# Optimization experiments

Hardware: AMD Instinct MI355X
Metric: run time of the kernel (lower is better)

## Reference

```python
import jax, jax.numpy as jnp
import numpy as np

N = 50000      # num nodes
E = 800000     # num edges (before self loops)
F_IN = 128     # fea_size
D = 128        # g_dim_per_layer[i]
H = 4          # heads
C = D // H     # out_channels per head
NEG_SLOPE = 0.2  # PyG GATConv default leaky_relu slope


def setup_inputs() -> dict:
    key = jax.random.key(0)
    ks = jax.random.split(key, 20)
    inp = {
        "x": jax.random.normal(ks[0], (N, F_IN), dtype=jnp.float32),
        "edge_index": jax.random.randint(ks[1], (2, E), 0, N, dtype=jnp.int32),
        "w0": jax.random.normal(ks[2], (F_IN, D), dtype=jnp.float32) * 0.05,
        "b0": jnp.zeros((D,), dtype=jnp.float32),
    }
    for i in (1, 2, 3):
        k = 4 * i
        inp[f"w{i}"] = jax.random.normal(ks[k], (D, D), dtype=jnp.float32) * 0.05
        inp[f"a_src{i}"] = jax.random.normal(ks[k + 1], (H, C), dtype=jnp.float32) * 0.1
        inp[f"a_dst{i}"] = jax.random.normal(ks[k + 2], (H, C), dtype=jnp.float32) * 0.1
        inp[f"b{i}"] = jnp.zeros((D,), dtype=jnp.float32)
    return inp


def _gat_layer(x, src, dst, w, a_src, a_dst, b):
    # PyG GATConv (eval mode, dropout inactive, add_self_loops already applied)
    n = x.shape[0]
    xp = (x @ w).reshape(n, H, C)                       # [N,H,C]
    al_s = jnp.einsum("nhc,hc->nh", xp, a_src)          # [N,H]
    al_d = jnp.einsum("nhc,hc->nh", xp, a_dst)          # [N,H]
    e = jax.nn.leaky_relu(al_s[src] + al_d[dst], NEG_SLOPE)  # [E',H]
    # softmax over incoming edges of each destination node
    m = jax.ops.segment_max(e, dst, num_segments=n)
    e = jnp.exp(e - m[dst])
    s = jax.ops.segment_sum(e, dst, num_segments=n)
    alpha = e / s[dst]                                  # [E',H]
    msg = alpha[:, :, None] * xp[src]                   # [E',H,C]
    out = jax.ops.segment_sum(msg, dst, num_segments=n)  # [N,H,C]
    return out.reshape(n, H * C) + b


def reference(x, edge_index, w0, b0, w1, a_src1, a_dst1, b1,
              w2, a_src2, a_dst2, b2, w3, a_src3, a_dst3, b3):
    n = x.shape[0]
    loops = jnp.arange(n, dtype=edge_index.dtype)
    ei = jnp.concatenate([edge_index, jnp.stack([loops, loops])], axis=1)
    src, dst = ei[0], ei[1]  # messages flow src -> dst (PyG convention)

    h = x @ w0 + b0
    h = jax.nn.relu(h + _gat_layer(h, src, dst, w1, a_src1, a_dst1, b1))
    h = jax.nn.relu(h + _gat_layer(h, src, dst, w2, a_src2, a_dst2, b2))
    return _gat_layer(h, src, dst, w3, a_src3, a_dst3, b3)
```

## Files before the change

kernel.cpp:

```cpp
#include <hip/hip_runtime.h>

#define F 128
#define HEADS 4
#define NEG 0.2f
#define CAP 128
#define CAPP 136
#define CB 6144

typedef unsigned short u16;
typedef unsigned int u32;
typedef __attribute__((ext_vector_type(8))) unsigned short us8;
typedef __attribute__((ext_vector_type(8))) short short8;
typedef __attribute__((ext_vector_type(4))) float f32x4;

__device__ __forceinline__ float bf2f(u16 u) {
  union { u32 i; float f; } v; v.i = ((u32)u) << 16; return v.f;
}
__device__ __forceinline__ float bflo(u32 p) {
  union { u32 i; float f; } v; v.i = p << 16; return v.f;
}
__device__ __forceinline__ float bfhi(u32 p) {
  union { u32 i; float f; } v; v.i = p & 0xFFFF0000u; return v.f;
}
__device__ __forceinline__ u16 f2bf(float f) {
  union { u32 i; float f; } v; v.f = f;
  if (((v.i >> 23) & 0xFF) == 0xFF) return 0;
  u32 r = v.i + 0x7FFF + ((v.i >> 16) & 1);
  return (u16)(r >> 16);
}
__device__ __forceinline__ float sane(float f) {
  union { u32 i; float f; } v; v.f = f;
  return (((v.i >> 23) & 0xFF) == 0xFF) ? 0.f : f;
}
__device__ __forceinline__ u16 bfsane(u16 u) {
  return (((u >> 7) & 0xFF) == 0xFF) ? (u16)0 : u;
}

__device__ __forceinline__ bool detect_f32_wave(const u16* __restrict__ p) {
  int lane = threadIdx.x & 63;
  const us8* q = (const us8*)p + lane * 4;
  int c = 0;
  #pragma unroll
  for (int k = 0; k < 4; k++) {
    us8 v = q[k];
    #pragma unroll
    for (int j = 0; j < 8; j++) { unsigned e = (v[j] >> 7) & 0xFF; c += (e >= 0xF8); }
  }
  #pragma unroll
  for (int off = 32; off; off >>= 1) c += __shfl_xor(c, off);
  return c > 4;
}

__global__ __launch_bounds__(256) void fill_const_bf16(u16* __restrict__ p, u16 v, int n) {
  int i = blockIdx.x * blockDim.x + threadIdx.x;
  if (i < n) p[i] = v;
}

__global__ __launch_bounds__(256) void setup(
    const void* w0, const void* w1, const void* w2, const void* w3,
    const void* b0, const void* b1, const void* b2, const void* b3,
    const void* as1, const void* ad1, const void* as2, const void* ad2,
    const void* as3, const void* ad3,
    u16* __restrict__ wsz, float* __restrict__ par,
    int* __restrict__ flg, int* __restrict__ gcur) {
  bool f32 = detect_f32_wave((const u16*)w0);
  int blk = blockIdx.x, tid = threadIdx.x;
  if (blk < 32) {
    int idx = blk * 256 + tid;
    int layer = idx >> 11;
    int rest  = idx & 2047;
    int lane = rest & 63;
    int ts   = rest >> 6;
    int s = ts & 3, t = ts >> 2;
    int kbase = s * 32 + (lane >> 4) * 8;
    int nn    = t * 16 + (lane & 15);
    const void* W = (layer == 0) ? w0 : (layer == 1) ? w1 : (layer == 2) ? w2 : w3;
    us8 o;
    #pragma unroll
    for (int j = 0; j < 8; j++) {
      int off = (kbase + j) * F + nn;
      o[j] = f32 ? f2bf(sane(((const float*)W)[off])) : bfsane(((const u16*)W)[off]);
    }
    *(us8*)(wsz + (size_t)idx * 8) = o;
  } else if (blk < 37) {
    int t = (blk - 32) * 256 + tid;
    if (t < 1280) {
      const void* tab[10] = {b0, b1, b2, b3, as1, ad1, as2, ad2, as3, ad3};
      const void* src = tab[t >> 7];
      int idx = t & 127;
      float v = f32 ? ((const float*)src)[idx] : bf2f(((const u16*)src)[idx]);
      par[t] = sane(v);
    }
  } else {
    gcur[tid] = 0;
    if (tid == 0) flg[0] = f32 ? 1 : 0;
  }
}

__global__ __launch_bounds__(256) void bucket_scatter(const int* __restrict__ ei,
                                                      int* __restrict__ gcur,
                                                      int2* __restrict__ ebuf,
                                                      int E, int E2, int n) {
  __shared__ int lcnt[256];
  __shared__ int gbase[256];
  int tid = threadIdx.x;
  lcnt[tid] = 0;
  __syncthreads();
  int srcv[16], dstv[16], rnk[16];
  #pragma unroll
  for (int i = 0; i < 16; i++) {
    int e = blockIdx.x * 4096 + i * 256 + tid;
    rnk[i] = -1;
    if (e < E2) {
      int src, dst;
      if (e < E) { src = ei[e]; dst = ei[E + e]; }
      else       { src = dst = e - E; }
      if ((unsigned)dst < (unsigned)n) {
        srcv[i] = src; dstv[i] = dst;
        rnk[i] = atomicAdd(&lcnt[dst >> 8], 1);
      }
    }
  }
  __syncthreads();
  int c = lcnt[tid];
  gbase[tid] = c ? atomicAdd(&gcur[tid], c) : 0;
  __syncthreads();
  #pragma unroll
  for (int i = 0; i < 16; i++) {
    if (rnk[i] >= 0) {
      int b = dstv[i] >> 8;
      int slot = gbase[b] + rnk[i];
      if (slot < CB) ebuf[(size_t)b * CB + slot] = make_int2(srcv[i], dstv[i]);
    }
  }
}

__global__ __launch_bounds__(256) void bucket_fill(const int* __restrict__ gcur,
                                                   const int2* __restrict__ ebuf,
                                                   int* __restrict__ rp,
                                                   int* __restrict__ col, int n) {
  __shared__ int sc[256];
  __shared__ int ncnt[256];
  __shared__ int nofs[256];
  __shared__ int wsums[4];
  __shared__ int total_s;
  int b = blockIdx.x, tid = threadIdx.x, lane = tid & 63, wv = tid >> 6;

  int v = min(gcur[tid], CB);
  int x = v;
  #pragma unroll
  for (int off = 1; off < 64; off <<= 1) {
    int t = __shfl_up(x, off);
    if (lane >= off) x += t;
  }
  if (lane == 63) wsums[wv] = x;
  __syncthreads();
  int add = 0;
  for (int w = 0; w < wv; w++) add += wsums[w];
  sc[tid] = add + x - v;
  if (tid == 255) total_s = add + x;
  __syncthreads();

  int tot = min(gcur[b], CB);
  int colbase = sc[b];
  const int2* eb = ebuf + (size_t)b * CB;
  ncnt[tid] = 0;
  __syncthreads();
  for (int j = tid; j < tot; j += 256) atomicAdd(&ncnt[eb[j].y & 255], 1);
  __syncthreads();
  v = ncnt[tid];
  x = v;
  #pragma unroll
  for (int off = 1; off < 64; off <<= 1) {
    int t = __shfl_up(x, off);
    if (lane >= off) x += t;
  }
  if (lane == 63) wsums[wv] = x;
  __syncthreads();
  add = 0;
  for (int w = 0; w < wv; w++) add += wsums[w];
  nofs[tid] = add + x - v;
  int node = (b << 8) + tid;
  if (node < n) rp[node] = colbase + nofs[tid];
  if (b == 0 && tid == 0) rp[n] = total_s;
  __syncthreads();
  ncnt[tid] = 0;
  __syncthreads();
  for (int j = tid; j < tot; j += 256) {
    int2 e = eb[j];
    int ln = e.y & 255;
    int r = atomicAdd(&ncnt[ln], 1);
    col[colbase + nofs[ln] + r] = e.x;
  }
}

__global__ __launch_bounds__(128) void gemm_mfma(
    const void* __restrict__ A, const u16* __restrict__ wszL,
    const float* __restrict__ biasc, const float* __restrict__ avec,
    u16* __restrict__ Cm, float* __restrict__ al_s, float* __restrict__ al_d,
    const int* __restrict__ flgp, int nrows, int a_src) {
  int tid = threadIdx.x, wv = tid >> 6, lane = tid & 63;
  int quad = lane >> 4, l15 = lane & 15;
  int m0 = blockIdx.x * 32 + wv * 16;
  int mrow = m0 + l15;
  int ml = mrow < nrows ? mrow : (nrows - 1);

  float asv[8], adv[8];
  if (avec) {
    #pragma unroll
    for (int t = 0; t < 8; t++) {
      asv[t] = avec[t * 16 + l15];
      adv[t] = avec[128 + t * 16 + l15];
    }
  }

  short8 af[4];
  if (a_src && flgp[0]) {
    const float* ar = (const float*)A + (size_t)ml * F;
    #pragma unroll
    for (int s = 0; s < 4; s++) {
      float4 u = *(const float4*)(ar + s * 32 + quad * 8);
      float4 v = *(const float4*)(ar + s * 32 + quad * 8 + 4);
      short8 p;
      p[0] = (short)f2bf(sane(u.x)); p[1] = (short)f2bf(sane(u.y));
      p[2] = (short)f2bf(sane(u.z)); p[3] = (short)f2bf(sane(u.w));
      p[4] = (short)f2bf(sane(v.x)); p[5] = (short)f2bf(sane(v.y));
      p[6] = (short)f2bf(sane(v.z)); p[7] = (short)f2bf(sane(v.w));
      af[s] = p;
    }
  } else {
    const u16* ar = (const u16*)A + (size_t)ml * F;
    #pragma unroll
    for (int s = 0; s < 4; s++) af[s] = *(const short8*)(ar + s * 32 + quad * 8);
  }

  f32x4 acc[8];
  #pragma unroll
  for (int t = 0; t < 8; t++) acc[t] = (f32x4){0.f, 0.f, 0.f, 0.f};
  #pragma unroll
  for (int s = 0; s < 4; s++) {
    #pragma unroll
    for (int t = 0; t < 8; t++) {
      short8 bf = *(const short8*)(wszL + (size_t)(((t << 2) | s) * 64 + lane) * 8);
      acc[t] = __builtin_amdgcn_mfma_f32_16x16x32_bf16(af[s], bf, acc[t], 0, 0, 0);
    }
  }

  float ps[4][4], pd[4][4];
  if (avec) {
    #pragma unroll
    for (int r = 0; r < 4; r++)
      #pragma unroll
      for (int h = 0; h < 4; h++) { ps[r][h] = 0.f; pd[r][h] = 0.f; }
  }

  #pragma unroll
  for (int t = 0; t < 8; t++) {
    int cc = t * 16 + l15;
    float b = biasc ? biasc[cc] : 0.f;
    int h = t >> 1;
    #pragma unroll
    for (int r = 0; r < 4; r++) {
      float v = sane(acc[t][r] + b);
      int row = m0 + quad * 4 + r;
      if (row < nrows) Cm[(size_t)row * F + cc] = f2bf(v);
      if (avec) { ps[r][h] += v * asv[t]; pd[r][h] += v * adv[t]; }
    }
  }

  if (avec) {
    #pragma unroll
    for (int r = 0; r < 4; r++)
      #pragma unroll
      for (int h = 0; h < 4; h++) {
        float a = ps[r][h], d = pd[r][h];
        #pragma unroll
        for (int off = 1; off < 16; off <<= 1) {
          a += __shfl_xor(a, off);
          d += __shfl_xor(d, off);
        }
        ps[r][h] = a; pd[r][h] = d;
      }
    if (l15 == 0) {
      #pragma unroll
      for (int r = 0; r < 4; r++) {
        int row = m0 + quad * 4 + r;
        if (row < nrows) {
          float4 vs = {sane(ps[r][0]), sane(ps[r][1]), sane(ps[r][2]), sane(ps[r][3])};
          float4 vd = {sane(pd[r][0]), sane(pd[r][1]), sane(pd[r][2]), sane(pd[r][3])};
          ((float4*)al_s)[row] = vs;
          ((float4*)al_d)[row] = vd;
        }
      }
    }
  }
}

__global__ __launch_bounds__(256) void gat_aggregate(
    const u16* __restrict__ xp, const float* __restrict__ al_s,
    const float* __restrict__ al_d, const int* __restrict__ row_ptr,
    const int* __restrict__ col, const float* __restrict__ biasc,
    u16* __restrict__ hio, const int* __restrict__ flgp,
    int n, int E2, int mode) {
  __shared__ int   sb[4][2][CAP];
  __shared__ float wb[4][2][4][CAPP];
  int tid = threadIdx.x;
  int wv = tid >> 6, lane = tid & 63;
  int half = lane >> 5, hl = lane & 31;
  int node = blockIdx.x * 8 + wv * 2 + half;
  bool active = node < n;
  int beg = 0, end = 0;
  float ald_[4] = {0.f, 0.f, 0.f, 0.f};
  if (active) {
    beg = row_ptr[node]; end = row_ptr[node + 1];
    if (beg < 0) beg = 0; if (beg > E2) beg = E2;
    if (end < beg) end = beg; if (end > E2) end = E2;
    float4 qd = ((const float4*)al_d)[node];
    ald_[0] = qd.x; ald_[1] = qd.y; ald_[2] = qd.z; ald_[3] = qd.w;
  }
  int deg = end - beg;
  int ch = hl * 4, head = hl >> 3;
  u32 cb = (u32)hl * 8;
  const char* xpb = (const char*)xp;
  float a0 = 0.f, a1 = 0.f, a2 = 0.f, a3 = 0.f;

  if (deg <= CAP) {
    float er[4][4];
    float m4[4] = {-1e30f, -1e30f, -1e30f, -1e30f};
    #pragma unroll
    for (int it = 0; it < 4; it++) {
      int jj = hl + it * 32;
      if (jj < deg) {
        int src = col[beg + jj];
        if ((unsigned)src >= (unsigned)n) src = node;
        sb[wv][half][jj] = src;
        float4 q = ((const float4*)al_s)[src];
        float as_[4] = {q.x, q.y, q.z, q.w};
        #pragma unroll
        for (int h = 0; h < 4; h++) {
          float e = as_[h] + ald_[h];
          e = (e > 0.f) ? e : NEG * e;
          er[it][h] = e;
          m4[h] = fmaxf(m4[h], e);
        }
      }
    }
    #pragma unroll
    for (int off = 16; off; off >>= 1)
      #pragma unroll
      for (int h = 0; h < 4; h++) m4[h] = fmaxf(m4[h], __shfl_xor(m4[h], off));
    float s4[4] = {0.f, 0.f, 0.f, 0.f};
    #pragma unroll
    for (int it = 0; it < 4; it++) {
      int jj = hl + it * 32;
      if (jj < deg) {
        #pragma unroll
        for (int h = 0; h < 4; h++) {
          float w = __expf(er[it][h] - m4[h]);
          s4[h] += w;
          wb[wv][half][h][jj] = w;
        }
      }
    }
    #pragma unroll
    for (int off = 16; off; off >>= 1)
      #pragma unroll
      for (int h = 0; h < 4; h++) s4[h] += __shfl_xor(s4[h], off);
    float inv = (s4[head] > 0.f) ? 1.f / s4[head] : 0.f;
    __asm__ volatile("s_waitcnt lgkmcnt(0)" ::: "memory");
    const int* srow = sb[wv][half];
    const float* wrow = wb[wv][half][head];
    int j = 0;
    for (; j + 4 <= deg; j += 4) {
      int4 sa = *(const int4*)(srow + j);
      float4 wa = *(const float4*)(wrow + j);
      uint2 p0 = *(const uint2*)(xpb + (((u32)sa.x << 8) + cb));
      uint2 p1 = *(const uint2*)(xpb + (((u32)sa.y << 8) + cb));
      uint2 p2 = *(const uint2*)(xpb + (((u32)sa.z << 8) + cb));
      uint2 p3 = *(const uint2*)(xpb + (((u32)sa.w << 8) + cb));
      a0 += wa.x * bflo(p0.x) + wa.y * bflo(p1.x) + wa.z * bflo(p2.x) + wa.w * bflo(p3.x);
      a1 += wa.x * bfhi(p0.x) + wa.y * bfhi(p1.x) + wa.z * bfhi(p2.x) + wa.w * bfhi(p3.x);
      a2 += wa.x * bflo(p0.y) + wa.y * bflo(p1.y) + wa.z * bflo(p2.y) + wa.w * bflo(p3.y);
      a3 += wa.x * bfhi(p0.y) + wa.y * bfhi(p1.y) + wa.z * bfhi(p2.y) + wa.w * bfhi(p3.y);
    }
    for (; j < deg; j++) {
      int s0 = srow[j];
      float w0 = wrow[j];
      uint2 p0 = *(const uint2*)(xpb + (((u32)s0 << 8) + cb));
      a0 += w0 * bflo(p0.x); a1 += w0 * bfhi(p0.x);
      a2 += w0 * bflo(p0.y); a3 += w0 * bfhi(p0.y);
    }
    a0 *= inv; a1 *= inv; a2 *= inv; a3 *= inv;
  } else {
    float m = -1.0e30f, s = 0.f;
    for (int j = beg; j < end; ++j) {
      int src = col[j];
      if ((unsigned)src >= (unsigned)n) continue;
      float e = al_s[src * 4 + head] + ald_[head];
      e = (e > 0.f) ? e : NEG * e;
      float mn = fmaxf(m, e);
      float scale = __expf(m - mn);
      float w = __expf(e - mn);
      uint2 pv = *(const uint2*)(xpb + (((u32)src << 8) + cb));
      s = s * scale + w;
      a0 = a0 * scale + w * bflo(pv.x);
      a1 = a1 * scale + w * bfhi(pv.x);
      a2 = a2 * scale + w * bflo(pv.y);
      a3 = a3 * scale + w * bfhi(pv.y);
      m = mn;
    }
    float inv = (s > 0.f) ? 1.f / s : 0.f;
    a0 *= inv; a1 *= inv; a2 *= inv; a3 *= inv;
  }

  if (!active) return;
  float4 b4 = *(const float4*)(biasc + ch);
  float o0 = sane(a0) + b4.x, o1 = sane(a1) + b4.y;
  float o2 = sane(a2) + b4.z, o3 = sane(a3) + b4.w;
  size_t o = (size_t)node * F + ch;
  if (mode == 0) {
    uint2 hv = *(const uint2*)(hio + o);
    o0 = fmaxf(bflo(hv.x) + o0, 0.f);
    o1 = fmaxf(bfhi(hv.x) + o1, 0.f);
    o2 = fmaxf(bflo(hv.y) + o2, 0.f);
    o3 = fmaxf(bfhi(hv.y) + o3, 0.f);
    uint2 st;
    st.x = ((u32)f2bf(sane(o1)) << 16) | (u32)f2bf(sane(o0));
    st.y = ((u32)f2bf(sane(o3)) << 16) | (u32)f2bf(sane(o2));
    *(uint2*)(hio + o) = st;
  } else {
    if (flgp[0]) {
      float4 st = {sane(o0), sane(o1), sane(o2), sane(o3)};
      *(float4*)((float*)hio + o) = st;
    } else {
      uint2 st;
      st.x = ((u32)f2bf(sane(o1)) << 16) | (u32)f2bf(sane(o0));
      st.y = ((u32)f2bf(sane(o3)) << 16) | (u32)f2bf(sane(o2));
      *(uint2*)(hio + o) = st;
    }
  }
}

extern "C" void kernel_launch(void* const* d_in, const int* in_sizes, int n_in,
                              void* d_out, int out_size, void* d_ws, size_t ws_size,
                              hipStream_t stream) {
  const int* ei = (const int*)d_in[1];

  const int N  = in_sizes[0] / F;
  const int E  = in_sizes[1] / 2;
  const int E2 = E + N;
  const int NB = (N + 255) >> 8;

  uintptr_t base = ((uintptr_t)d_ws + 255) & ~(uintptr_t)255;
  size_t off_par = 0;
  size_t off_flg = off_par + (size_t)1536 * 4;
  size_t off_wsz = off_flg + 256;
  size_t off_xp  = off_wsz + (size_t)65536 * 2;
  size_t off_als = off_xp  + (size_t)N * F * 2;
  size_t off_ald = off_als + (size_t)N * HEADS * 4;
  size_t off_gc  = off_ald + (size_t)N * HEADS * 4;
  size_t off_rp  = off_gc  + 1024;
  size_t off_col = off_rp  + (size_t)(N + 1) * 4;
  size_t off_eb  = (off_col + (size_t)E2 * 4 + 255) & ~(size_t)255;
  size_t need    = off_eb + (size_t)NB * CB * 8 + 512 + ((uintptr_t)d_ws & 255);

  if (ws_size < need) {
    fill_const_bf16<<<(out_size + 255) / 256, 256, 0, stream>>>(
        (u16*)d_out, (u16)0x4316, out_size);
    return;
  }

  float* par   = (float*)(base + off_par);
  int* flg     = (int*)(base + off_flg);
  u16* wsz     = (u16*)(base + off_wsz);
  u16* xp      = (u16*)(base + off_xp);
  float* al_s  = (float*)(base + off_als);
  float* al_d  = (float*)(base + off_ald);
  int* gcur    = (int*)(base + off_gc);
  int* row_ptr = (int*)(base + off_rp);
  int* col     = (int*)(base + off_col);
  int2* ebuf   = (int2*)(base + off_eb);

  float* bc[4];
  for (int l = 0; l < 4; ++l) bc[l] = par + (size_t)l * 128;
  float* avec[3];
  for (int l = 0; l < 3; ++l) avec[l] = par + 512 + (size_t)l * 256;

  u16* hio = (u16*)d_out;

  setup<<<38, 256, 0, stream>>>(
      d_in[2], d_in[4], d_in[8], d_in[12],
      d_in[3], d_in[7], d_in[11], d_in[15],
      d_in[5], d_in[6], d_in[9], d_in[10], d_in[13], d_in[14],
      wsz, par, flg, gcur);

  bucket_scatter<<<(E2 + 4095) / 4096, 256, 0, stream>>>(ei, gcur, ebuf, E, E2, N);
  bucket_fill<<<NB, 256, 0, stream>>>(gcur, ebuf, row_ptr, col, N);

  const int GB = (N + 31) / 32;
  gemm_mfma<<<GB, 128, 0, stream>>>(d_in[0], wsz, bc[0], nullptr, hio,
                                    al_s, al_d, flg, N, 1);

  for (int l = 0; l < 3; ++l) {
    gemm_mfma<<<GB, 128, 0, stream>>>(hio, wsz + (size_t)(l + 1) * 16384, nullptr,
                                      avec[l], xp, al_s, al_d, flg, N, 0);
    gat_aggregate<<<(N + 7) / 8, 256, 0, stream>>>(
        xp, al_s, al_d, row_ptr, col, bc[l + 1], hio, flg, N, E2, (l < 2) ? 0 : 1);
  }
}
```

Before: 324.9 us.

## Fuse graph build with GEMMs, fold attention vectors into MFMA, prefetch gather

Precomputes W·a_src and W·a_dst per layer in setup so the attention logits come from an extra MFMA column tile instead of a shuffle reduction in the GEMM epilogue. Runs the edge bucket scatter and the first projection GEMM in one launch, and the CSR fill and the layer-1 GEMM in another, so independent work overlaps and fewer kernels are launched. The aggregation inner loop also software-prefetches the next four neighbor rows. The cost is heavier setup work, plus logits rounded through bf16 weight vectors and possible load imbalance inside the merged grids.

```diff
diff --git a/kernel.cpp b/kernel.cpp
--- a/kernel.cpp
+++ b/kernel.cpp
@@ -61,8 +61,9 @@
     const void* b0, const void* b1, const void* b2, const void* b3,
     const void* as1, const void* ad1, const void* as2, const void* ad2,
     const void* as3, const void* ad3,
-    u16* __restrict__ wsz, float* __restrict__ par,
+    u16* __restrict__ wsz, u16* __restrict__ avf, float* __restrict__ par,
     int* __restrict__ flg, int* __restrict__ gcur) {
+  __shared__ float vv[8][128];
   bool f32 = detect_f32_wave((const u16*)w0);
   int blk = blockIdx.x, tid = threadIdx.x;
   if (blk < 32) {
@@ -91,16 +92,112 @@
       float v = f32 ? ((const float*)src)[idx] : bf2f(((const u16*)src)[idx]);
       par[t] = sane(v);
     }
-  } else {
+  } else if (blk == 37) {
     gcur[tid] = 0;
     if (tid == 0) flg[0] = f32 ? 1 : 0;
-  }
-}
-
-__global__ __launch_bounds__(256) void bucket_scatter(const int* __restrict__ ei,
-                                                      int* __restrict__ gcur,
-                                                      int2* __restrict__ ebuf,
-                                                      int E, int E2, int n) {
+  } else {
+    int l = blk - 38;
+    const void* W   = (l == 0) ? w1 : (l == 1) ? w2 : w3;
+    const void* asp = (l == 0) ? as1 : (l == 1) ? as2 : as3;
+    const void* adp = (l == 0) ? ad1 : (l == 1) ? ad2 : ad3;
+    for (int e = tid; e < 1024; e += 256) {
+      int vec = e >> 7, k = e & 127;
+      int h = vec & 3;
+      const void* av = (vec < 4) ? asp : adp;
+      float sum = 0.f;
+      for (int c = 0; c < 32; c++) {
+        int col = h * 32 + c;
+        float wv_ = f32 ? ((const float*)W)[k * F + col] : bf2f(((const u16*)W)[k * F + col]);
+        float aa  = f32 ? ((const float*)av)[col]        : bf2f(((const u16*)av)[col]);
+        sum += sane(wv_) * sane(aa);
+      }
+      vv[vec][k] = sane(sum);
+    }
+    __syncthreads();
+    int s = tid >> 6, lane = tid & 63;
+    int quad = lane >> 4, l15 = lane & 15;
+    int kbase = s * 32 + quad * 8;
+    us8 o;
+    #pragma unroll
+    for (int j = 0; j < 8; j++)
+      o[j] = (l15 < 8) ? f2bf(vv[l15][kbase + j]) : (u16)0;
+    *(us8*)(avf + (((size_t)l * 4 + s) * 64 + lane) * 8) = o;
+  }
+}
+
+__device__ __forceinline__ void gemm_tile(
+    int m0, int lane, const void* __restrict__ A, int f32in,
+    const u16* __restrict__ wszL, const float* __restrict__ biasc,
+    const u16* __restrict__ avfL, u16* __restrict__ Cm,
+    float* __restrict__ al_s, float* __restrict__ al_d, int nrows) {
+  int quad = lane >> 4, l15 = lane & 15;
+  int mrow = m0 + l15;
+  int ml = mrow < nrows ? mrow : (nrows - 1);
+  short8 af[4];
+  if (f32in) {
+    const float* ar = (const float*)A + (size_t)ml * F;
+    #pragma unroll
+    for (int s = 0; s < 4; s++) {
+      float4 u = *(const float4*)(ar + s * 32 + quad * 8);
+      float4 v = *(const float4*)(ar + s * 32 + quad * 8 + 4);
+      short8 p;
+      p[0] = (short)f2bf(sane(u.x)); p[1] = (short)f2bf(sane(u.y));
+      p[2] = (short)f2bf(sane(u.z)); p[3] = (short)f2bf(sane(u.w));
+      p[4] = (short)f2bf(sane(v.x)); p[5] = (short)f2bf(sane(v.y));
+      p[6] = (short)f2bf(sane(v.z)); p[7] = (short)f2bf(sane(v.w));
+      af[s] = p;
+    }
+  } else {
+    const u16* ar = (const u16*)A + (size_t)ml * F;
+    #pragma unroll
+    for (int s = 0; s < 4; s++) af[s] = *(const short8*)(ar + s * 32 + quad * 8);
+  }
+
+  f32x4 acc[8];
+  #pragma unroll
+  for (int t = 0; t < 8; t++) acc[t] = (f32x4){0.f, 0.f, 0.f, 0.f};
+  f32x4 accL = (f32x4){0.f, 0.f, 0.f, 0.f};
+
+  #pragma unroll
+  for (int s = 0; s < 4; s++) {
+    short8 bfr[8];
+    #pragma unroll
+    for (int t = 0; t < 8; t++)
+      bfr[t] = *(const short8*)(wszL + (size_t)(((t << 2) | s) * 64 + lane) * 8);
+    if (avfL) {
+      short8 av = *(const short8*)(avfL + (size_t)(s * 64 + lane) * 8);
+      accL = __builtin_amdgcn_mfma_f32_16x16x32_bf16(af[s], av, accL, 0, 0, 0);
+    }
+    #pragma unroll
+    for (int t = 0; t < 8; t++)
+      acc[t] = __builtin_amdgcn_mfma_f32_16x16x32_bf16(af[s], bfr[t], acc[t], 0, 0, 0);
+  }
+
+  #pragma unroll
+  for (int t = 0; t < 8; t++) {
+    int cc = t * 16 + l15;
+    float b = biasc ? biasc[cc] : 0.f;
+    #pragma unroll
+    for (int r = 0; r < 4; r++) {
+      int row = m0 + quad * 4 + r;
+      if (row < nrows) Cm[(size_t)row * F + cc] = f2bf(sane(acc[t][r] + b));
+    }
+  }
+  if (avfL && l15 < 8) {
+    float* dst = (l15 < 4) ? al_s : al_d;
+    int h = l15 & 3;
+    #pragma unroll
+    for (int r = 0; r < 4; r++) {
+      int row = m0 + quad * 4 + r;
+      if (row < nrows) dst[(size_t)row * 4 + h] = sane(accL[r]);
+    }
+  }
+}
+
+__device__ __forceinline__ void scatter_body(const int* __restrict__ ei,
+                                             int* __restrict__ gcur,
+                                             int2* __restrict__ ebuf,
+                                             int E, int E2, int n, int blk) {
   __shared__ int lcnt[256];
   __shared__ int gbase[256];
   int tid = threadIdx.x;
@@ -109,7 +206,7 @@
   int srcv[16], dstv[16], rnk[16];
   #pragma unroll
   for (int i = 0; i < 16; i++) {
-    int e = blockIdx.x * 4096 + i * 256 + tid;
+    int e = blk * 4096 + i * 256 + tid;
     rnk[i] = -1;
     if (e < E2) {
       int src, dst;
@@ -135,17 +232,16 @@
   }
 }
 
-__global__ __launch_bounds__(256) void bucket_fill(const int* __restrict__ gcur,
-                                                   const int2* __restrict__ ebuf,
-                                                   int* __restrict__ rp,
-                                                   int* __restrict__ col, int n) {
+__device__ __forceinline__ void fill_body(const int* __restrict__ gcur,
+                                          const int2* __restrict__ ebuf,
+                                          int* __restrict__ rp,
+                                          int* __restrict__ col, int n, int b) {
   __shared__ int sc[256];
   __shared__ int ncnt[256];
   __shared__ int nofs[256];
   __shared__ int wsums[4];
   __shared__ int total_s;
-  int b = blockIdx.x, tid = threadIdx.x, lane = tid & 63, wv = tid >> 6;
-
+  int tid = threadIdx.x, lane = tid & 63, wv = tid >> 6;
   int v = min(gcur[tid], CB);
   int x = v;
   #pragma unroll
@@ -160,7 +256,6 @@
   sc[tid] = add + x - v;
   if (tid == 255) total_s = add + x;
   __syncthreads();
-
   int tot = min(gcur[b], CB);
   int colbase = sc[b];
   const int2* eb = ebuf + (size_t)b * CB;
@@ -194,106 +289,45 @@
   }
 }
 
-__global__ __launch_bounds__(128) void gemm_mfma(
+__global__ __launch_bounds__(256) void scatter_gemm0(
+    const int* __restrict__ ei, int* __restrict__ gcur, int2* __restrict__ ebuf,
+    int E, int E2, int n, int SB,
+    const void* __restrict__ x, const int* __restrict__ flg,
+    const u16* __restrict__ wsz, const float* __restrict__ b0c,
+    u16* __restrict__ hio) {
+  int blk = blockIdx.x;
+  if (blk < SB) {
+    scatter_body(ei, gcur, ebuf, E, E2, n, blk);
+  } else {
+    int tid = threadIdx.x, wv = tid >> 6, lane = tid & 63;
+    int m0 = (blk - SB) * 64 + wv * 16;
+    gemm_tile(m0, lane, x, flg[0], wsz, b0c, nullptr, hio, nullptr, nullptr, n);
+  }
+}
+
+__global__ __launch_bounds__(256) void fill_gemm1(
+    const int* __restrict__ gcur, const int2* __restrict__ ebuf,
+    int* __restrict__ rp, int* __restrict__ col, int n, int NBv,
+    const void* __restrict__ hA, const u16* __restrict__ wszL,
+    const u16* __restrict__ avfL, u16* __restrict__ xp,
+    float* __restrict__ al_s, float* __restrict__ al_d) {
+  int blk = blockIdx.x;
+  if (blk < NBv) {
+    fill_body(gcur, ebuf, rp, col, n, blk);
+  } else {
+    int tid = threadIdx.x, wv = tid >> 6, lane = tid & 63;
+    int m0 = (blk - NBv) * 64 + wv * 16;
+    gemm_tile(m0, lane, hA, 0, wszL, nullptr, avfL, xp, al_s, al_d, n);
+  }
+}
+
+__global__ __launch_bounds__(128) void gemm_std(
     const void* __restrict__ A, const u16* __restrict__ wszL,
-    const float* __restrict__ biasc, const float* __restrict__ avec,
-    u16* __restrict__ Cm, float* __restrict__ al_s, float* __restrict__ al_d,
-    const int* __restrict__ flgp, int nrows, int a_src) {
+    const u16* __restrict__ avfL, u16* __restrict__ Cm,
+    float* __restrict__ al_s, float* __restrict__ al_d, int nrows) {
   int tid = threadIdx.x, wv = tid >> 6, lane = tid & 63;
-  int quad = lane >> 4, l15 = lane & 15;
   int m0 = blockIdx.x * 32 + wv * 16;
-  int mrow = m0 + l15;
-  int ml = mrow < nrows ? mrow : (nrows - 1);
-
-  float asv[8], adv[8];
-  if (avec) {
-    #pragma unroll
-    for (int t = 0; t < 8; t++) {
-      asv[t] = avec[t * 16 + l15];
-      adv[t] = avec[128 + t * 16 + l15];
-    }
-  }
-
-  short8 af[4];
-  if (a_src && flgp[0]) {
-    const float* ar = (const float*)A + (size_t)ml * F;
-    #pragma unroll
-    for (int s = 0; s < 4; s++) {
-      float4 u = *(const float4*)(ar + s * 32 + quad * 8);
-      float4 v = *(const float4*)(ar + s * 32 + quad * 8 + 4);
-      short8 p;
-      p[0] = (short)f2bf(sane(u.x)); p[1] = (short)f2bf(sane(u.y));
-      p[2] = (short)f2bf(sane(u.z)); p[3] = (short)f2bf(sane(u.w));
-      p[4] = (short)f2bf(sane(v.x)); p[5] = (short)f2bf(sane(v.y));
-      p[6] = (short)f2bf(sane(v.z)); p[7] = (short)f2bf(sane(v.w));
-      af[s] = p;
-    }
-  } else {
-    const u16* ar = (const u16*)A + (size_t)ml * F;
-    #pragma unroll
-    for (int s = 0; s < 4; s++) af[s] = *(const short8*)(ar + s * 32 + quad * 8);
-  }
-
-  f32x4 acc[8];
-  #pragma unroll
-  for (int t = 0; t < 8; t++) acc[t] = (f32x4){0.f, 0.f, 0.f, 0.f};
-  #pragma unroll
-  for (int s = 0; s < 4; s++) {
-    #pragma unroll
-    for (int t = 0; t < 8; t++) {
-      short8 bf = *(const short8*)(wszL + (size_t)(((t << 2) | s) * 64 + lane) * 8);
-      acc[t] = __builtin_amdgcn_mfma_f32_16x16x32_bf16(af[s], bf, acc[t], 0, 0, 0);
-    }
-  }
-
-  float ps[4][4], pd[4][4];
-  if (avec) {
-    #pragma unroll
-    for (int r = 0; r < 4; r++)
-      #pragma unroll
-      for (int h = 0; h < 4; h++) { ps[r][h] = 0.f; pd[r][h] = 0.f; }
-  }
-
-  #pragma unroll
-  for (int t = 0; t < 8; t++) {
-    int cc = t * 16 + l15;
-    float b = biasc ? biasc[cc] : 0.f;
-    int h = t >> 1;
-    #pragma unroll
-    for (int r = 0; r < 4; r++) {
-      float v = sane(acc[t][r] + b);
-      int row = m0 + quad * 4 + r;
-      if (row < nrows) Cm[(size_t)row * F + cc] = f2bf(v);
-      if (avec) { ps[r][h] += v * asv[t]; pd[r][h] += v * adv[t]; }
-    }
-  }
-
-  if (avec) {
-    #pragma unroll
-    for (int r = 0; r < 4; r++)
-      #pragma unroll
-      for (int h = 0; h < 4; h++) {
-        float a = ps[r][h], d = pd[r][h];
-        #pragma unroll
-        for (int off = 1; off < 16; off <<= 1) {
-          a += __shfl_xor(a, off);
-          d += __shfl_xor(d, off);
-        }
-        ps[r][h] = a; pd[r][h] = d;
-      }
-    if (l15 == 0) {
-      #pragma unroll
-      for (int r = 0; r < 4; r++) {
-        int row = m0 + quad * 4 + r;
-        if (row < nrows) {
-          float4 vs = {sane(ps[r][0]), sane(ps[r][1]), sane(ps[r][2]), sane(ps[r][3])};
-          float4 vd = {sane(pd[r][0]), sane(pd[r][1]), sane(pd[r][2]), sane(pd[r][3])};
-          ((float4*)al_s)[row] = vs;
-          ((float4*)al_d)[row] = vd;
-        }
-      }
-    }
-  }
+  gemm_tile(m0, lane, A, 0, wszL, nullptr, avfL, Cm, al_s, al_d, nrows);
 }
 
 __global__ __launch_bounds__(256) void gat_aggregate(
@@ -371,17 +405,31 @@
     const int* srow = sb[wv][half];
     const float* wrow = wb[wv][half][head];
     int j = 0;
-    for (; j + 4 <= deg; j += 4) {
-      int4 sa = *(const int4*)(srow + j);
-      float4 wa = *(const float4*)(wrow + j);
-      uint2 p0 = *(const uint2*)(xpb + (((u32)sa.x << 8) + cb));
-      uint2 p1 = *(const uint2*)(xpb + (((u32)sa.y << 8) + cb));
-      uint2 p2 = *(const uint2*)(xpb + (((u32)sa.z << 8) + cb));
-      uint2 p3 = *(const uint2*)(xpb + (((u32)sa.w << 8) + cb));
-      a0 += wa.x * bflo(p0.x) + wa.y * bflo(p1.x) + wa.z * bflo(p2.x) + wa.w * bflo(p3.x);
-      a1 += wa.x * bfhi(p0.x) + wa.y * bfhi(p1.x) + wa.z * bfhi(p2.x) + wa.w * bfhi(p3.x);
-      a2 += wa.x * bflo(p0.y) + wa.y * bflo(p1.y) + wa.z * bflo(p2.y) + wa.w * bflo(p3.y);
-      a3 += wa.x * bfhi(p0.y) + wa.y * bfhi(p1.y) + wa.z * bfhi(p2.y) + wa.w * bfhi(p3.y);
+    if (deg >= 4) {
+      int4 sa = *(const int4*)(srow);
+      float4 wa = *(const float4*)(wrow);
+      uint2 P0 = *(const uint2*)(xpb + (((u32)sa.x << 8) + cb));
+      uint2 P1 = *(const uint2*)(xpb + (((u32)sa.y << 8) + cb));
+      uint2 P2 = *(const uint2*)(xpb + (((u32)sa.z << 8) + cb));
+      uint2 P3 = *(const uint2*)(xpb + (((u32)sa.w << 8) + cb));
+      for (; j + 8 <= deg; j += 4) {
+        int4 sn = *(const int4*)(srow + j + 4);
+        float4 wn = *(const float4*)(wrow + j + 4);
+        uint2 Q0 = *(const uint2*)(xpb + (((u32)sn.x << 8) + cb));
+        uint2 Q1 = *(const uint2*)(xpb + (((u32)sn.y << 8) + cb));
+        uint2 Q2 = *(const uint2*)(xpb + (((u32)sn.z << 8) + cb));
+        uint2 Q3 = *(const uint2*)(xpb + (((u32)sn.w << 8) + cb));
+        a0 += wa.x * bflo(P0.x) + wa.y * bflo(P1.x) + wa.z * bflo(P2.x) + wa.w * bflo(P3.x);
+        a1 += wa.x * bfhi(P0.x) + wa.y * bfhi(P1.x) + wa.z * bfhi(P2.x) + wa.w * bfhi(P3.x);
+        a2 += wa.x * bflo(P0.y) + wa.y * bflo(P1.y) + wa.z * bflo(P2.y) + wa.w * bflo(P3.y);
+        a3 += wa.x * bfhi(P0.y) + wa.y * bfhi(P1.y) + wa.z * bfhi(P2.y) + wa.w * bfhi(P3.y);
+        wa = wn; P0 = Q0; P1 = Q1; P2 = Q2; P3 = Q3;
+      }
+      a0 += wa.x * bflo(P0.x) + wa.y * bflo(P1.x) + wa.z * bflo(P2.x) + wa.w * bflo(P3.x);
+      a1 += wa.x * bfhi(P0.x) + wa.y * bfhi(P1.x) + wa.z * bfhi(P2.x) + wa.w * bfhi(P3.x);
+      a2 += wa.x * bflo(P0.y) + wa.y * bflo(P1.y) + wa.z * bflo(P2.y) + wa.w * bflo(P3.y);
+      a3 += wa.x * bfhi(P0.y) + wa.y * bfhi(P1.y) + wa.z * bfhi(P2.y) + wa.w * bfhi(P3.y);
+      j += 4;
     }
     for (; j < deg; j++) {
       int s0 = srow[j];
@@ -450,12 +498,16 @@
   const int E  = in_sizes[1] / 2;
   const int E2 = E + N;
   const int NB = (N + 255) >> 8;
+  const int SB = (E2 + 4095) / 4096;
+  const int GB64  = (N + 63) / 64;
+  const int GB128 = (N + 31) / 32;
 
   uintptr_t base = ((uintptr_t)d_ws + 255) & ~(uintptr_t)255;
   size_t off_par = 0;
   size_t off_flg = off_par + (size_t)1536 * 4;
   size_t off_wsz = off_flg + 256;
-  size_t off_xp  = off_wsz + (size_t)65536 * 2;
+  size_t off_avf = off_wsz + (size_t)65536 * 2;
+  size_t off_xp  = off_avf + (size_t)6144 * 2;
   size_t off_als = off_xp  + (size_t)N * F * 2;
   size_t off_ald = off_als + (size_t)N * HEADS * 4;
   size_t off_gc  = off_ald + (size_t)N * HEADS * 4;
@@ -473,6 +525,7 @@
   float* par   = (float*)(base + off_par);
   int* flg     = (int*)(base + off_flg);
   u16* wsz     = (u16*)(base + off_wsz);
+  u16* avf     = (u16*)(base + off_avf);
   u16* xp      = (u16*)(base + off_xp);
   float* al_s  = (float*)(base + off_als);
   float* al_d  = (float*)(base + off_ald);
@@ -483,28 +536,30 @@
 
   float* bc[4];
   for (int l = 0; l < 4; ++l) bc[l] = par + (size_t)l * 128;
-  float* avec[3];
-  for (int l = 0; l < 3; ++l) avec[l] = par + 512 + (size_t)l * 256;
 
   u16* hio = (u16*)d_out;
 
-  setup<<<38, 256, 0, stream>>>(
+  setup<<<41, 256, 0, stream>>>(
       d_in[2], d_in[4], d_in[8], d_in[12],
       d_in[3], d_in[7], d_in[11], d_in[15],
       d_in[5], d_in[6], d_in[9], d_in[10], d_in[13], d_in[14],
-      wsz, par, flg, gcur);
-
-  bucket_scatter<<<(E2 + 4095) / 4096, 256, 0, stream>>>(ei, gcur, ebuf, E, E2, N);
-  bucket_fill<<<NB, 256, 0, stream>>>(gcur, ebuf, row_ptr, col, N);
-
-  const int GB = (N + 31) / 32;
-  gemm_mfma<<<GB, 128, 0, stream>>>(d_in[0], wsz, bc[0], nullptr, hio,
-                                    al_s, al_d, flg, N, 1);
-
-  for (int l = 0; l < 3; ++l) {
-    gemm_mfma<<<GB, 128, 0, stream>>>(hio, wsz + (size_t)(l + 1) * 16384, nullptr,
-                                      avec[l], xp, al_s, al_d, flg, N, 0);
-    gat_aggregate<<<(N + 7) / 8, 256, 0, stream>>>(
-        xp, al_s, al_d, row_ptr, col, bc[l + 1], hio, flg, N, E2, (l < 2) ? 0 : 1);
-  }
-}
+      wsz, avf, par, flg, gcur);
+
+  scatter_gemm0<<<SB + GB64, 256, 0, stream>>>(
+      ei, gcur, ebuf, E, E2, N, SB, d_in[0], flg, wsz, bc[0], hio);
+
+  fill_gemm1<<<NB + GB64, 256, 0, stream>>>(
+      gcur, ebuf, row_ptr, col, N, NB,
+      hio, wsz + (size_t)1 * 16384, avf, xp, al_s, al_d);
+
+  gat_aggregate<<<(N + 7) / 8, 256, 0, stream>>>(
+      xp, al_s, al_d, row_ptr, col, bc[1], hio, flg, N, E2, 0);
+  gemm_std<<<GB128, 128, 0, stream>>>(hio, wsz + (size_t)2 * 16384,
+                                      avf + (size_t)1 * 2048, xp, al_s, al_d, N);
+  gat_aggregate<<<(N + 7) / 8, 256, 0, stream>>>(
+      xp, al_s, al_d, row_ptr, col, bc[2], hio, flg, N, E2, 0);
+  gemm_std<<<GB128, 128, 0, stream>>>(hio, wsz + (size_t)3 * 16384,
+                                      avf + (size_t)2 * 2048, xp, al_s, al_d, N);
+  gat_aggregate<<<(N + 7) / 8, 256, 0, stream>>>(
+      xp, al_s, al_d, row_ptr, col, bc[3], hio, flg, N, E2, 1);
+}
```

Result: faster. 304.4 us (-6.3%).
